# Performance work log

Hardware: AMD Instinct MI355X
Metric: run time of the kernel (lower is better)

The kernel has to match this reference:

```python
import jax, jax.numpy as jnp
import numpy as np

N_HEAD = 16


def setup_inputs() -> dict:
    key = jax.random.key(0)
    ks = jax.random.split(key, 5)
    B, T, C = 4, 2048, 1024
    s = 0.02
    x = jax.random.normal(ks[0], (B, T, C), jnp.float32)
    wq = jax.random.normal(ks[1], (C, C), jnp.float32) * s
    wk = jax.random.normal(ks[2], (C, C), jnp.float32) * s
    wv = jax.random.normal(ks[3], (C, C), jnp.float32) * s
    wp = jax.random.normal(ks[4], (C, C), jnp.float32) * s
    zb = jnp.zeros((C,), jnp.float32)
    return {"x": x, "wq": wq, "bq": zb, "wk": wk, "bk": zb,
            "wv": wv, "bv": zb, "wp": wp, "bp": zb}


def _rope_cos_sin(T, D):
    half = D // 2
    i = jnp.arange(half, dtype=jnp.float32)
    alpha = 1.0 / (10000.0 ** (2.0 * i / D))        # [half]
    ang = jnp.arange(T, dtype=jnp.float32)[:, None] * alpha  # [T, half]
    return jnp.cos(ang), jnp.sin(ang)


def _apply_rope(t, cos, sin):
    # t: [B, H, T, D]; non-interleaved halves as in the torch module
    half = t.shape[-1] // 2
    xr, xi = t[..., :half], t[..., half:]
    return jnp.concatenate([xr * cos - xi * sin, xr * sin + xi * cos], axis=-1)


def reference(x, wq, bq, wk, bk, wv, bv, wp, bp):
    B, T, C = x.shape
    H = N_HEAD
    D = C // H
    # QKV projections (torch Linear: x @ W.T + b)
    def heads(w, b):
        return (x @ w.T + b).reshape(B, T, H, D).transpose(0, 2, 1, 3)
    q, k, v = heads(wq, bq), heads(wk, bk), heads(wv, bv)
    cos, sin = _rope_cos_sin(T, D)  # each [T, D//2], broadcasts over B,H
    q = _apply_rope(q, cos, sin)
    k = _apply_rope(k, cos, sin)
    scale = 1.0 / np.sqrt(D).astype(np.float32)
    att = jnp.einsum('bhtd,bhsd->bhts', q, k) * scale  # [B,H,T,T]
    causal = jnp.tril(jnp.ones((T, T), bool))
    att = jnp.where(causal, att, jnp.float32(-jnp.inf))
    att = jax.nn.softmax(att, axis=-1)
    y = jnp.einsum('bhts,bhsd->bhtd', att, v)  # [B,H,T,D]
    y = y.transpose(0, 2, 1, 3).reshape(B, T, C)
    return y @ wp.T + bp
```

## Files before the change

### kernel.cpp

```cpp
#include <hip/hip_runtime.h>
#include <math.h>

constexpr int B = 4, T = 2048, C = 1024, H = 16, D = 64;
constexpr int M = B * T;
constexpr size_t BTC = (size_t)B * T * C;
constexpr float QSCALE = 0.18033688011112042f;
constexpr float ROPE_C = -0.415241011861f;

typedef short bf16x8 __attribute__((ext_vector_type(8)));
typedef float f32x4 __attribute__((ext_vector_type(4)));

__device__ inline ushort f2bf(float f) {
  union { float f; unsigned u; } cv; cv.f = f;
  unsigned u = cv.u;
  u += 0x7fffu + ((u >> 16) & 1u);
  return (ushort)(u >> 16);
}
__device__ inline ushort f2bfr(float f) {
  union { float f; unsigned u; } cv; cv.f = f;
  return (ushort)((cv.u + 0x8000u) >> 16);
}

__device__ inline void async_load16(const void* g, void* l) {
  __builtin_amdgcn_global_load_lds(
      (const __attribute__((address_space(1))) void*)g,
      (__attribute__((address_space(3))) void*)l, 16, 0, 0);
}

__device__ __forceinline__ bf16x8 ones_frag() {
  bf16x8 v;
#pragma unroll
  for (int i = 0; i < 8; i++) v[i] = (short)0x3F80;
  return v;
}

__global__ __launch_bounds__(256) void conv_all(
    const float* __restrict__ x, const float* __restrict__ w0,
    const float* __restrict__ w1, const float* __restrict__ w2,
    const float* __restrict__ w3, ushort* __restrict__ xb,
    ushort* __restrict__ wb) {
  const int XBLK = (int)(BTC / 1024);
  const int WBLK = (C * C) / 1024;
  int blk = blockIdx.x;
  const float* src;
  ushort* dst;
  int i;
  if (blk < XBLK) {
    src = x; dst = xb;
    i = (blk * 256 + threadIdx.x) * 4;
  } else {
    int wseg = (blk - XBLK) >> 10;
    int wblk = (blk - XBLK) & (WBLK - 1);
    src = (wseg == 0) ? w0 : (wseg == 1) ? w1 : (wseg == 2) ? w2 : w3;
    dst = wb + (size_t)wseg * C * C;
    i = (wblk * 256 + threadIdx.x) * 4;
  }
  float4 v = *(const float4*)(src + i);
  ushort4 o;
  o.x = f2bf(v.x); o.y = f2bf(v.y); o.z = f2bf(v.z); o.w = f2bf(v.w);
  *(ushort4*)(dst + i) = o;
}

constexpr int QNT = C / 64;

template <int OM, int NCT>
__global__ __launch_bounds__(256, 2) void gemm_pipe(
    const ushort* __restrict__ A, const ushort* __restrict__ Wt,
    const float* __restrict__ b0, const float* __restrict__ b1,
    const float* __restrict__ b2, void* __restrict__ out1,
    void* __restrict__ out2, void* __restrict__ out3) {
  __shared__ ushort As[2][128 * 64] __attribute__((aligned(16)));
  __shared__ ushort Bs[3][128 * 64] __attribute__((aligned(16)));
  const int tid = threadIdx.x;
  const int lane = tid & 63;
  const int lrow = lane & 15, quad = lane >> 4;
  const int wave = tid >> 6;
  const int wr = wave >> 1, wc = wave & 1;
  const int x7 = lrow & 7;

  int bid = blockIdx.y * NCT + blockIdx.x;
  const int cpx = NCT * 8;
  int lin = (bid & 7) * cpx + (bid >> 3);
  int row0 = (lin / NCT) * 128;
  int col0 = (lin % NCT) * 128;

  unsigned gaA[4], gaB[4];
#pragma unroll
  for (int i = 0; i < 4; i++) {
    int c = tid + i * 256;
    int r = c >> 3, cl = c & 7;
    int g = (cl ^ (r & 7)) * 8;
    gaA[i] = (unsigned)(row0 + r) * C + g;
    gaB[i] = (unsigned)(col0 + r) * C + g;
  }

  f32x4 acc[4][4];
#pragma unroll
  for (int i = 0; i < 4; i++)
#pragma unroll
    for (int j = 0; j < 4; j++) acc[i][j] = (f32x4){0.f, 0.f, 0.f, 0.f};

#pragma unroll
  for (int i = 0; i < 4; i++)
    async_load16(A + gaA[i], &As[0][(tid + i * 256) * 8]);
#pragma unroll
  for (int i = 0; i < 4; i++)
    async_load16(Wt + gaB[i], &Bs[0][(tid + i * 256) * 8]);
#pragma unroll
  for (int i = 0; i < 4; i++)
    async_load16(Wt + gaB[i] + 64, &Bs[1][(tid + i * 256) * 8]);
  asm volatile("s_waitcnt vmcnt(4)" ::: "memory");
  __builtin_amdgcn_sched_barrier(0);
  __builtin_amdgcn_s_barrier();

  int bi = 0;
  for (int t = 0; t < QNT; ++t) {
    const int pa = t & 1;
    const ushort* Ap = As[pa];
    const ushort* Bp = Bs[bi];
    int bi2 = bi - 1; if (bi2 < 0) bi2 = 2;

    {
      const int slot = (quad ^ x7) * 8;
      bf16x8 aF[4], bF[4];
#pragma unroll
      for (int i = 0; i < 4; i++)
        aF[i] = *(const bf16x8*)&Ap[(wr * 64 + i * 16 + lrow) * 64 + slot];
#pragma unroll
      for (int j = 0; j < 4; j++)
        bF[j] = *(const bf16x8*)&Bp[(wc * 64 + j * 16 + lrow) * 64 + slot];
      if (t + 1 < QNT) {
#pragma unroll
        for (int i = 0; i < 4; i++)
          async_load16(A + gaA[i] + (t + 1) * 64,
                       &As[pa ^ 1][(tid + i * 256) * 8]);
      }
      __builtin_amdgcn_s_setprio(1);
#pragma unroll
      for (int i = 0; i < 4; i++)
#pragma unroll
        for (int j = 0; j < 4; j++)
          acc[i][j] = __builtin_amdgcn_mfma_f32_16x16x32_bf16(
              aF[i], bF[j], acc[i][j], 0, 0, 0);
      __builtin_amdgcn_s_setprio(0);
    }

    {
      const int slot = ((4 + quad) ^ x7) * 8;
      bf16x8 aF[4], bF[4];
#pragma unroll
      for (int i = 0; i < 4; i++)
        aF[i] = *(const bf16x8*)&Ap[(wr * 64 + i * 16 + lrow) * 64 + slot];
#pragma unroll
      for (int j = 0; j < 4; j++)
        bF[j] = *(const bf16x8*)&Bp[(wc * 64 + j * 16 + lrow) * 64 + slot];
      if (t + 2 < QNT) {
#pragma unroll
        for (int i = 0; i < 4; i++)
          async_load16(Wt + gaB[i] + (t + 2) * 64,
                       &Bs[bi2][(tid + i * 256) * 8]);
      }
      __builtin_amdgcn_s_setprio(1);
#pragma unroll
      for (int i = 0; i < 4; i++)
#pragma unroll
        for (int j = 0; j < 4; j++)
          acc[i][j] = __builtin_amdgcn_mfma_f32_16x16x32_bf16(
              aF[i], bF[j], acc[i][j], 0, 0, 0);
      __builtin_amdgcn_s_setprio(0);
    }

    if (t + 2 < QNT) {
      asm volatile("s_waitcnt vmcnt(4)" ::: "memory");
    } else {
      asm volatile("s_waitcnt vmcnt(0)" ::: "memory");
    }
    __builtin_amdgcn_sched_barrier(0);
    __builtin_amdgcn_s_barrier();
    bi = (bi == 2) ? 0 : bi + 1;
  }

  const int nb = col0 + wc * 64;
  const int mbase = row0 + wr * 64;
  const float* bias = (col0 < 1024) ? b0 : (col0 < 2048) ? b1 : b2;
  float bn[4];
#pragma unroll
  for (int j = 0; j < 4; j++) bn[j] = bias[(nb & 1023) + j * 16 + lrow];

  if (OM == 0) {
    const int N = C;
    float* outp = (float*)out1;
#pragma unroll
    for (int i = 0; i < 4; i++)
#pragma unroll
      for (int j = 0; j < 4; j++) {
        int n = nb + j * 16 + lrow;
#pragma unroll
        for (int r = 0; r < 4; r++) {
          int m = mbase + i * 16 + quad * 4 + r;
          outp[(size_t)m * N + n] = acc[i][j][r] + bn[j];
        }
      }
  } else {
    int seg = nb >> 10;
    int hh = (nb & 1023) >> 6;
    if (seg < 2) {
      ushort* dst = (seg == 0) ? (ushort*)out1 : (ushort*)out2;
      float scale = (seg == 0) ? QSCALE : 1.0f;
      float a0 = __builtin_amdgcn_exp2f((float)lrow * ROPE_C);
      float a1 = __builtin_amdgcn_exp2f((float)(lrow + 16) * ROPE_C);
#pragma unroll
      for (int i = 0; i < 4; i++) {
#pragma unroll
        for (int r = 0; r < 4; r++) {
          int m = mbase + i * 16 + quad * 4 + r;
          int tt = m & (T - 1), bb = m >> 11;
          float s0, c0, s1, c1;
          __sincosf((float)tt * a0, &s0, &c0);
          __sincosf((float)tt * a1, &s1, &c1);
          float xr0 = acc[i][0][r] + bn[0];
          float xi0 = acc[i][2][r] + bn[2];
          float xr1 = acc[i][1][r] + bn[1];
          float xi1 = acc[i][3][r] + bn[3];
          ushort* pp = dst + ((size_t)(bb * H + hh) * T + tt) * D + lrow;
          pp[0]  = f2bf((xr0 * c0 - xi0 * s0) * scale);
          pp[32] = f2bf((xr0 * s0 + xi0 * c0) * scale);
          pp[16] = f2bf((xr1 * c1 - xi1 * s1) * scale);
          pp[48] = f2bf((xr1 * s1 + xi1 * c1) * scale);
        }
      }
    } else {
      ushort* dst = (ushort*)out3;
#pragma unroll
      for (int i = 0; i < 4; i++) {
        int m0 = mbase + i * 16 + quad * 4;
        int t0 = m0 & (T - 1), bb = m0 >> 11;
        size_t base = (size_t)(bb * H + hh) * D * T + t0;
#pragma unroll
        for (int j = 0; j < 4; j++) {
          int d = j * 16 + lrow;
          ushort4 pk;
          pk.x = f2bf(acc[i][j][0] + bn[j]);
          pk.y = f2bf(acc[i][j][1] + bn[j]);
          pk.z = f2bf(acc[i][j][2] + bn[j]);
          pk.w = f2bf(acc[i][j][3] + bn[j]);
          *(ushort4*)(dst + base + (size_t)d * T) = pk;
        }
      }
    }
  }
}

__device__ __forceinline__ void stage_kv(
    const ushort* kbh, const ushort* vbh, int s0,
    ushort* Kl, ushort* Vl, int tid) {
#pragma unroll
  for (int i = 0; i < 2; i++) {
    int c = tid + i * 256;
    int r = c >> 3, cc = c & 7;
    int g = (cc ^ (r & 7)) * 8;
    async_load16(kbh + (size_t)(s0 + r) * D + g, Kl + c * 8);
    async_load16(vbh + (size_t)r * T + s0 + g, Vl + c * 8);
  }
}

template <int MODE>
__device__ __forceinline__ void attn_step4(
    int s0, const ushort* KL, const ushort* VL, ushort* P,
    const bf16x8 (&qf)[2][2], int lrow, int quad, int sw0, int sw1,
    int qg0, int qg1, f32x4 (&o)[4][2], f32x4 (&ol)[2]) {
  bf16x8 kf0[4], kf1[4];
#pragma unroll
  for (int kt = 0; kt < 4; kt++) {
    int base = (kt * 16 + lrow) * 64;
    kf0[kt] = *(const bf16x8*)&KL[base + sw0];
    kf1[kt] = *(const bf16x8*)&KL[base + sw1];
  }
  bf16x8 vf0[4], vf1[4];
#pragma unroll
  for (int ds = 0; ds < 4; ds++) {
    int base = (ds * 16 + lrow) * 64;
    vf0[ds] = *(const bf16x8*)&VL[base + sw0];
    vf1[ds] = *(const bf16x8*)&VL[base + sw1];
  }
#pragma unroll
  for (int g = 0; g < 2; g++) {
    if (MODE == 2 && g == 0) continue;
    int qg = g ? qg1 : qg0;
    f32x4 st[4];
#pragma unroll
    for (int kt = 0; kt < 4; kt++) {
      f32x4 z = {0.f, 0.f, 0.f, 0.f};
      st[kt] = __builtin_amdgcn_mfma_f32_16x16x32_bf16(kf0[kt], qf[g][0], z, 0, 0, 0);
      st[kt] = __builtin_amdgcn_mfma_f32_16x16x32_bf16(kf1[kt], qf[g][1], st[kt], 0, 0, 0);
    }
    if ((MODE == 1 && g == 0) || (MODE == 2 && g == 1)) {
#pragma unroll
      for (int kt = 0; kt < 4; kt++)
#pragma unroll
        for (int r = 0; r < 4; r++)
          if (s0 + kt * 16 + quad * 4 + r > qg) st[kt][r] = -1e30f;
    }
#pragma unroll
    for (int kt = 0; kt < 4; kt++) {
      ushort4 pk;
      pk.x = f2bfr(__builtin_amdgcn_exp2f(st[kt][0]));
      pk.y = f2bfr(__builtin_amdgcn_exp2f(st[kt][1]));
      pk.z = f2bfr(__builtin_amdgcn_exp2f(st[kt][2]));
      pk.w = f2bfr(__builtin_amdgcn_exp2f(st[kt][3]));
      *(ushort4*)&P[((2 * kt + (quad >> 1)) * 32 + g * 16 + lrow) * 8 + (quad & 1) * 4] = pk;
    }
  }
  asm volatile("" ::: "memory");
  bf16x8 ones = ones_frag();
#pragma unroll
  for (int g = 0; g < 2; g++) {
    if (MODE == 2 && g == 0) continue;
    bf16x8 pf0 = *(const bf16x8*)&P[(quad * 32 + g * 16 + lrow) * 8];
    bf16x8 pf1 = *(const bf16x8*)&P[((quad + 4) * 32 + g * 16 + lrow) * 8];
    ol[g] = __builtin_amdgcn_mfma_f32_16x16x32_bf16(ones, pf0, ol[g], 0, 0, 0);
    ol[g] = __builtin_amdgcn_mfma_f32_16x16x32_bf16(ones, pf1, ol[g], 0, 0, 0);
#pragma unroll
    for (int ds = 0; ds < 4; ds++) {
      o[ds][g] = __builtin_amdgcn_mfma_f32_16x16x32_bf16(vf0[ds], pf0, o[ds][g], 0, 0, 0);
      o[ds][g] = __builtin_amdgcn_mfma_f32_16x16x32_bf16(vf1[ds], pf1, o[ds][g], 0, 0, 0);
    }
  }
}

__global__ __launch_bounds__(256, 3) void attn_mfma4(
    const ushort* __restrict__ qb_, const ushort* __restrict__ kb_,
    const ushort* __restrict__ vtb_, ushort* __restrict__ y) {
  __shared__ ushort Kl[2][64 * 64] __attribute__((aligned(16)));
  __shared__ ushort Vl[2][64 * 64] __attribute__((aligned(16)));
  __shared__ ushort Pl[4][2048] __attribute__((aligned(16)));
  int tid = threadIdx.x;
  int wave = tid >> 6, lane = tid & 63;
  int lrow = lane & 15, quad = lane >> 4;
  int qbi = 15 - (int)(blockIdx.x >> 6);
  int bh = blockIdx.x & 63;
  int b = bh >> 4, h = bh & 15;
  int Q0 = qbi * 128;
  ushort* P = Pl[wave];
  const ushort* kbh = kb_ + (size_t)bh * T * D;
  const ushort* vbh = vtb_ + (size_t)bh * D * T;

  int qg0 = Q0 + wave * 16 + lrow;
  int qg1 = qg0 + 64;
  bf16x8 qf[2][2];
  {
    const ushort* qp0 = qb_ + ((size_t)bh * T + qg0) * D + quad * 8;
    qf[0][0] = *(const bf16x8*)qp0;
    qf[0][1] = *(const bf16x8*)(qp0 + 32);
    const ushort* qp1 = qb_ + ((size_t)bh * T + qg1) * D + quad * 8;
    qf[1][0] = *(const bf16x8*)qp1;
    qf[1][1] = *(const bf16x8*)(qp1 + 32);
  }
  int r7 = lrow & 7;
  int sw0 = (quad ^ r7) * 8;
  int sw1 = ((quad + 4) ^ r7) * 8;

  f32x4 o[4][2];
#pragma unroll
  for (int ds = 0; ds < 4; ds++)
#pragma unroll
    for (int g = 0; g < 2; g++) o[ds][g] = (f32x4){0.f, 0.f, 0.f, 0.f};
  f32x4 ol[2] = {(f32x4){0.f, 0.f, 0.f, 0.f}, (f32x4){0.f, 0.f, 0.f, 0.f}};

  int trips = 2 * qbi + 2;
  stage_kv(kbh, vbh, 0, Kl[0], Vl[0], tid);
  int it = 0;
  for (; it < trips - 2; ++it) {
    __syncthreads();
    stage_kv(kbh, vbh, (it + 1) * 64, Kl[(it + 1) & 1], Vl[(it + 1) & 1], tid);
    attn_step4<0>(it * 64, Kl[it & 1], Vl[it & 1], P, qf, lrow, quad, sw0, sw1,
                  qg0, qg1, o, ol);
  }
  __syncthreads();
  stage_kv(kbh, vbh, (it + 1) * 64, Kl[(it + 1) & 1], Vl[(it + 1) & 1], tid);
  attn_step4<1>(it * 64, Kl[it & 1], Vl[it & 1], P, qf, lrow, quad, sw0, sw1,
                qg0, qg1, o, ol);
  ++it;
  __syncthreads();
  attn_step4<2>(it * 64, Kl[it & 1], Vl[it & 1], P, qf, lrow, quad, sw0, sw1,
                qg0, qg1, o, ol);

#pragma unroll
  for (int g = 0; g < 2; g++) {
    float inv = 1.f / ol[g][0];
    int qg = g ? qg1 : qg0;
#pragma unroll
    for (int ds = 0; ds < 4; ds++) {
      ushort4 pk;
      pk.x = f2bf(o[ds][g][0] * inv);
      pk.y = f2bf(o[ds][g][1] * inv);
      pk.z = f2bf(o[ds][g][2] * inv);
      pk.w = f2bf(o[ds][g][3] * inv);
      *(ushort4*)(y + ((size_t)b * T + qg) * C + h * D + ds * 16 + quad * 4) = pk;
    }
  }
}

extern "C" void kernel_launch(void* const* d_in, const int* in_sizes, int n_in,
                              void* d_out, int out_size, void* d_ws, size_t ws_size,
                              hipStream_t stream) {
  const float* x  = (const float*)d_in[0];
  const float* wq = (const float*)d_in[1];
  const float* bq = (const float*)d_in[2];
  const float* wk = (const float*)d_in[3];
  const float* bk = (const float*)d_in[4];
  const float* wv = (const float*)d_in[5];
  const float* bv = (const float*)d_in[6];
  const float* wp = (const float*)d_in[7];
  const float* bp = (const float*)d_in[8];
  float* out = (float*)d_out;

  ushort* xb    = (ushort*)d_ws;
  ushort* qb    = xb + BTC;
  ushort* kb    = qb + BTC;
  ushort* vtb   = kb + BTC;
  ushort* yb    = vtb + BTC;
  ushort* wqkvb = yb + BTC;
  ushort* wpb   = wqkvb + (size_t)3 * C * C;

  conv_all<<<(int)(BTC / 1024) + 4 * (C * C) / 1024, 256, 0, stream>>>(
      x, wq, wk, wv, wp, xb, wqkvb);

  dim3 qkv_grid(3 * C / 128, M / 128);
  gemm_pipe<1, 24><<<qkv_grid, 256, 0, stream>>>(
      xb, wqkvb, bq, bk, bv, qb, kb, vtb);

  attn_mfma4<<<(B * H * T / 128), 256, 0, stream>>>(qb, kb, vtb, yb);

  dim3 proj_grid(C / 128, M / 128);
  gemm_pipe<0, 8><<<proj_grid, 256, 0, stream>>>(
      yb, wpb, bp, bp, bp, out, nullptr, nullptr);
}
```

Baseline: 236.3 us.

## Load V fragments directly from global memory and raise MFMA wave priority

V tiles are no longer staged through LDS. Each wave now reads its V^T fragments straight from global memory into registers at the start of each step, while only K stays on the double-buffered async LDS path. This cuts LDS traffic and capacity, which may allow more blocks per CU, and s_setprio is wrapped around the MFMA sections to favour matrix issue. In exchange, the global V loads sit on the critical path with no prefetch, and every wave re-reads the same V data, leaning on the cache for latency.

Result: slower. 260.9 us (+10.4%).

```diff
diff --git a/kernel.cpp b/kernel.cpp
--- a/kernel.cpp
+++ b/kernel.cpp
@@ -251,24 +251,29 @@
   }
 }
 
-__device__ __forceinline__ void stage_kv(
-    const ushort* kbh, const ushort* vbh, int s0,
-    ushort* Kl, ushort* Vl, int tid) {
+__device__ __forceinline__ void stage_k(
+    const ushort* kbh, int s0, ushort* Kl, int tid) {
 #pragma unroll
   for (int i = 0; i < 2; i++) {
     int c = tid + i * 256;
     int r = c >> 3, cc = c & 7;
     int g = (cc ^ (r & 7)) * 8;
     async_load16(kbh + (size_t)(s0 + r) * D + g, Kl + c * 8);
-    async_load16(vbh + (size_t)r * T + s0 + g, Vl + c * 8);
   }
 }
 
 template <int MODE>
 __device__ __forceinline__ void attn_step4(
-    int s0, const ushort* KL, const ushort* VL, ushort* P,
+    int s0, const ushort* KL, const ushort* __restrict__ vbh, ushort* P,
     const bf16x8 (&qf)[2][2], int lrow, int quad, int sw0, int sw1,
     int qg0, int qg1, f32x4 (&o)[4][2], f32x4 (&ol)[2]) {
+  bf16x8 vf0[4], vf1[4];
+#pragma unroll
+  for (int ds = 0; ds < 4; ds++) {
+    const ushort* vp = vbh + (size_t)(ds * 16 + lrow) * T + s0 + quad * 8;
+    vf0[ds] = *(const bf16x8*)vp;
+    vf1[ds] = *(const bf16x8*)(vp + 32);
+  }
   bf16x8 kf0[4], kf1[4];
 #pragma unroll
   for (int kt = 0; kt < 4; kt++) {
@@ -276,24 +281,19 @@
     kf0[kt] = *(const bf16x8*)&KL[base + sw0];
     kf1[kt] = *(const bf16x8*)&KL[base + sw1];
   }
-  bf16x8 vf0[4], vf1[4];
-#pragma unroll
-  for (int ds = 0; ds < 4; ds++) {
-    int base = (ds * 16 + lrow) * 64;
-    vf0[ds] = *(const bf16x8*)&VL[base + sw0];
-    vf1[ds] = *(const bf16x8*)&VL[base + sw1];
-  }
 #pragma unroll
   for (int g = 0; g < 2; g++) {
     if (MODE == 2 && g == 0) continue;
     int qg = g ? qg1 : qg0;
     f32x4 st[4];
+    __builtin_amdgcn_s_setprio(1);
 #pragma unroll
     for (int kt = 0; kt < 4; kt++) {
       f32x4 z = {0.f, 0.f, 0.f, 0.f};
       st[kt] = __builtin_amdgcn_mfma_f32_16x16x32_bf16(kf0[kt], qf[g][0], z, 0, 0, 0);
       st[kt] = __builtin_amdgcn_mfma_f32_16x16x32_bf16(kf1[kt], qf[g][1], st[kt], 0, 0, 0);
     }
+    __builtin_amdgcn_s_setprio(0);
     if ((MODE == 1 && g == 0) || (MODE == 2 && g == 1)) {
 #pragma unroll
       for (int kt = 0; kt < 4; kt++)
@@ -318,6 +318,7 @@
     if (MODE == 2 && g == 0) continue;
     bf16x8 pf0 = *(const bf16x8*)&P[(quad * 32 + g * 16 + lrow) * 8];
     bf16x8 pf1 = *(const bf16x8*)&P[((quad + 4) * 32 + g * 16 + lrow) * 8];
+    __builtin_amdgcn_s_setprio(1);
     ol[g] = __builtin_amdgcn_mfma_f32_16x16x32_bf16(ones, pf0, ol[g], 0, 0, 0);
     ol[g] = __builtin_amdgcn_mfma_f32_16x16x32_bf16(ones, pf1, ol[g], 0, 0, 0);
 #pragma unroll
@@ -325,6 +326,7 @@
       o[ds][g] = __builtin_amdgcn_mfma_f32_16x16x32_bf16(vf0[ds], pf0, o[ds][g], 0, 0, 0);
       o[ds][g] = __builtin_amdgcn_mfma_f32_16x16x32_bf16(vf1[ds], pf1, o[ds][g], 0, 0, 0);
     }
+    __builtin_amdgcn_s_setprio(0);
   }
 }
 
@@ -332,7 +334,6 @@
     const ushort* __restrict__ qb_, const ushort* __restrict__ kb_,
     const ushort* __restrict__ vtb_, ushort* __restrict__ y) {
   __shared__ ushort Kl[2][64 * 64] __attribute__((aligned(16)));
-  __shared__ ushort Vl[2][64 * 64] __attribute__((aligned(16)));
   __shared__ ushort Pl[4][2048] __attribute__((aligned(16)));
   int tid = threadIdx.x;
   int wave = tid >> 6, lane = tid & 63;
@@ -368,21 +369,21 @@
   f32x4 ol[2] = {(f32x4){0.f, 0.f, 0.f, 0.f}, (f32x4){0.f, 0.f, 0.f, 0.f}};
 
   int trips = 2 * qbi + 2;
-  stage_kv(kbh, vbh, 0, Kl[0], Vl[0], tid);
+  stage_k(kbh, 0, Kl[0], tid);
   int it = 0;
   for (; it < trips - 2; ++it) {
     __syncthreads();
-    stage_kv(kbh, vbh, (it + 1) * 64, Kl[(it + 1) & 1], Vl[(it + 1) & 1], tid);
-    attn_step4<0>(it * 64, Kl[it & 1], Vl[it & 1], P, qf, lrow, quad, sw0, sw1,
+    stage_k(kbh, (it + 1) * 64, Kl[(it + 1) & 1], tid);
+    attn_step4<0>(it * 64, Kl[it & 1], vbh, P, qf, lrow, quad, sw0, sw1,
                   qg0, qg1, o, ol);
   }
   __syncthreads();
-  stage_kv(kbh, vbh, (it + 1) * 64, Kl[(it + 1) & 1], Vl[(it + 1) & 1], tid);
-  attn_step4<1>(it * 64, Kl[it & 1], Vl[it & 1], P, qf, lrow, quad, sw0, sw1,
+  stage_k(kbh, (it + 1) * 64, Kl[(it + 1) & 1], tid);
+  attn_step4<1>(it * 64, Kl[it & 1], vbh, P, qf, lrow, quad, sw0, sw1,
                 qg0, qg1, o, ol);
   ++it;
   __syncthreads();
-  attn_step4<2>(it * 64, Kl[it & 1], Vl[it & 1], P, qf, lrow, quad, sw0, sw1,
+  attn_step4<2>(it * 64, Kl[it & 1], vbh, P, qf, lrow, quad, sw0, sw1,
                 qg0, qg1, o, ol);
 
 #pragma unroll
```
